# Optimization experiments

Measured on AMD Instinct MI355X. Metric: run time of the kernel, lower is better.

## Reference

```python
import jax, jax.numpy as jnp
import numpy as np

D = 1024  # in_features == latent_dim
EPS = 1e-5


def _layernorm(x, g, b):
    mu = jnp.mean(x, axis=-1, keepdims=True)
    var = jnp.mean(jnp.square(x - mu), axis=-1, keepdims=True)
    return (x - mu) * jax.lax.rsqrt(var + EPS) * g + b


def setup_inputs() -> dict:
    key = jax.random.key(0)
    ks = jax.random.split(key, 8)
    s = 1.0 / np.sqrt(D)
    return {
        "x": jax.random.normal(ks[0], (4, 4096, D), dtype=jnp.float32),
        "w_qkv": jax.random.uniform(ks[1], (3 * D, D), jnp.float32, -s, s),
        "w_o": jax.random.uniform(ks[2], (D, D), jnp.float32, -s, s),
        "w1": jax.random.uniform(ks[3], (D, D), jnp.float32, -s, s),
        "b1": jax.random.uniform(ks[4], (D,), jnp.float32, -s, s),
        "w2": jax.random.uniform(ks[5], (D, D), jnp.float32, -s, s),
        "b2": jax.random.uniform(ks[6], (D,), jnp.float32, -s, s),
        "ln1_g": jnp.ones((D,), jnp.float32),
        "ln1_b": jnp.zeros((D,), jnp.float32),
        "ln2_g": jnp.ones((D,), jnp.float32),
        "ln2_b": jnp.zeros((D,), jnp.float32),
    }


def reference(x, w_qkv, w_o, w1, b1, w2, b2, ln1_g, ln1_b, ln2_g, ln2_b):
    B, S, _ = x.shape
    scale = 1.0 / np.sqrt(D * 1)  # 1/sqrt(latent_dim * n_heads), n_heads=1
    qkv = jnp.einsum("bsd,ed->bse", x, w_qkv)            # [B,S,3D]
    qkv = qkv.reshape(B, S, 1, 3 * D).transpose(0, 2, 1, 3)  # [B,1,S,3D]
    q, k, v = jnp.split(qkv, 3, axis=-1)                  # each [B,1,S,D]
    logits = jnp.einsum("bhid,bhjd->bhij", q, k) * scale  # [B,1,S,S]
    # Faithful quirk: softmax over the HEAD axis (dim=1). With 1 head this
    # yields an all-ones attention matrix.
    attn = jax.nn.softmax(logits, axis=1)
    vals = jnp.einsum("bhij,bhjd->bhid", attn, v)         # [B,1,S,D]
    vals = vals.transpose(0, 2, 1, 3).reshape(B, S, D)
    attn_out = jnp.einsum("bsd,ed->bse", vals, w_o)
    # squeeze(-2) is a no-op for S>1
    x = _layernorm(x + attn_out, ln1_g, ln1_b)
    h = jax.nn.gelu(jnp.einsum("bsd,ed->bse", x, w1) + b1, approximate=False)
    mlp_out = jnp.einsum("bsd,ed->bse", h, w2) + b2
    return _layernorm(x + mlp_out, ln2_g, ln2_b)
```

## Files before the change

### kernel.cpp

```cpp
#include <hip/hip_runtime.h>
#include <hip/hip_bf16.h>

typedef __hip_bfloat16 bf16;
typedef __attribute__((ext_vector_type(8))) short short8;
typedef __attribute__((ext_vector_type(4))) float f32x4;

#define DDIM 1024
#define SEQ  4096
#define NB   4
#define MTOT (NB*SEQ)

static __device__ __forceinline__ unsigned short f2bf(float f) {
    __hip_bfloat16 h = __float2bfloat16(f);
    unsigned short u; __builtin_memcpy(&u, &h, 2); return u;
}
static __device__ __forceinline__ float bf2f(unsigned short u) {
    __hip_bfloat16 h; __builtin_memcpy(&h, &u, 2); return __bfloat162float(h);
}

__global__ __launch_bounds__(256) void pack_w_kernel(
    const float* __restrict__ w1, const float* __restrict__ w2,
    short8* __restrict__ w1p, short8* __restrict__ w2p)
{
    int gid  = blockIdx.x*256 + threadIdx.x;
    int m    = gid >> 17;
    int id   = gid & 131071;
    int frag = id >> 6, lane = id & 63;
    int ntile = frag >> 5, kt32 = frag & 31;
    int n = ntile*16 + (lane & 15);
    int k = kt32*32 + (lane >> 4)*8;
    const float* src = (m ? w2 : w1) + (size_t)n*DDIM + k;
    float4 a = *(const float4*)src;
    float4 b = *(const float4*)(src + 4);
    short8 o;
    o[0]=(short)f2bf(a.x); o[1]=(short)f2bf(a.y); o[2]=(short)f2bf(a.z); o[3]=(short)f2bf(a.w);
    o[4]=(short)f2bf(b.x); o[5]=(short)f2bf(b.y); o[6]=(short)f2bf(b.z); o[7]=(short)f2bf(b.w);
    (m ? w2p : w1p)[id] = o;
}

__global__ __launch_bounds__(256) void colsum_partial_kernel(
    const float* __restrict__ x, float* __restrict__ partial)
{
    int d  = blockIdx.x*256 + threadIdx.x;
    int b  = blockIdx.y;
    int sl = blockIdx.z;
    const float* p = x + ((size_t)b*SEQ + (size_t)sl*128)*DDIM + d;
    float s = 0.f;
    #pragma unroll 4
    for (int i = 0; i < 128; ++i) s += p[(size_t)i*DDIM];
    partial[((size_t)sl*NB + b)*DDIM + d] = s;
}

__global__ __launch_bounds__(256) void colsum_reduce_kernel(
    const float* __restrict__ partial, float* __restrict__ xsum)
{
    int d = blockIdx.x*256 + threadIdx.x;
    int b = blockIdx.y;
    float s = 0.f;
    #pragma unroll
    for (int sl = 0; sl < 32; ++sl) s += partial[((size_t)sl*NB + b)*DDIM + d];
    xsum[b*DDIM + d] = s;
}

__global__ __launch_bounds__(256) void matvec_kernel(
    const float* __restrict__ W, const float* __restrict__ vin, float* __restrict__ vout)
{
    int b = blockIdx.y;
    int g = threadIdx.x >> 4;
    int t = threadIdx.x & 15;
    int e = blockIdx.x*16 + g;
    const float* w = W + (size_t)e*DDIM;
    const float* v = vin + b*DDIM;
    float s = 0.f;
    for (int k = t; k < DDIM; k += 16) s += w[k]*v[k];
    #pragma unroll
    for (int o = 8; o; o >>= 1) s += __shfl_down(s, o, 16);
    if (t == 0) vout[b*DDIM + e] = s;
}

__global__ __launch_bounds__(256) void ln1_kernel(
    const float* __restrict__ x, const float* __restrict__ avec,
    const float* __restrict__ g1, const float* __restrict__ b1,
    unsigned short* __restrict__ x1b)
{
    int row = blockIdx.x;
    int b   = row >> 12;
    int tid = threadIdx.x;
    const float4* xr = (const float4*)(x + (size_t)row*DDIM);
    const float4* av = (const float4*)(avec + (size_t)b*DDIM);
    float4 xv = xr[tid], a4 = av[tid];
    float y0 = xv.x+a4.x, y1 = xv.y+a4.y, y2 = xv.z+a4.z, y3 = xv.w+a4.w;
    float s  = y0+y1+y2+y3;
    float ss = y0*y0+y1*y1+y2*y2+y3*y3;
    #pragma unroll
    for (int o = 32; o; o >>= 1) { s += __shfl_down(s,o,64); ss += __shfl_down(ss,o,64); }
    __shared__ float red[8];
    if ((tid&63) == 0) { red[tid>>6] = s; red[4+(tid>>6)] = ss; }
    __syncthreads();
    float St = red[0]+red[1]+red[2]+red[3];
    float Sq = red[4]+red[5]+red[6]+red[7];
    float mu = St*(1.0f/DDIM);
    float rs = rsqrtf(Sq*(1.0f/DDIM) - mu*mu + 1e-5f);
    float4 g4 = ((const float4*)g1)[tid];
    float4 bb = ((const float4*)b1)[tid];
    ushort4 o;
    o.x = f2bf((y0-mu)*rs*g4.x + bb.x);
    o.y = f2bf((y1-mu)*rs*g4.y + bb.y);
    o.z = f2bf((y2-mu)*rs*g4.z + bb.z);
    o.w = f2bf((y3-mu)*rs*g4.w + bb.w);
    *(ushort4*)(x1b + (size_t)row*DDIM + tid*4) = o;
}

template<int MODE>
__global__ __launch_bounds__(256, 2) void gemm_bp_kernel(
    const bf16* __restrict__ A, const short8* __restrict__ Bp,
    const float* __restrict__ bias, const unsigned short* __restrict__ resid,
    unsigned short* __restrict__ outb, float* __restrict__ outf)
{
    constexpr int K = 1024, N = 1024, BK = 64, NT = K / BK;
    __shared__ __align__(16) bf16 lds[2][128*BK];
    const int tid  = threadIdx.x;
    const int wave = tid >> 6, lane = tid & 63;

    int bid = blockIdx.x;
    int swz = (bid & 7) * 128 + (bid >> 3);
    const size_t bm = (size_t)(swz >> 3) * 128;
    const size_t bn = (size_t)(swz & 7) * 128;

    const int wm = wave >> 1;
    const int wn = wave & 1;

    const int srow = tid >> 3;
    const int skel = (((tid & 7) ^ ((tid >> 3) & 7)) << 3);

    const int fr = lane & 15;
    const int fs = lane >> 4;
    int foff[2];
    #pragma unroll
    for (int ks = 0; ks < 2; ++ks)
        foff[ks] = fr*128 + (((ks*4 + fs) ^ (fr & 7)) << 4);

    const bf16* Ab = A + bm * K;
    const int nt0 = (int)(bn >> 4) + wn*4;

    auto stageA = [&](int b, int kt) {
        #pragma unroll
        for (int g = 0; g < 4; ++g) {
            const bf16* gp = Ab + (size_t)(g*32 + srow) * K + kt*BK + skel;
            __builtin_amdgcn_global_load_lds(
                (const __attribute__((address_space(1))) void*)gp,
                (__attribute__((address_space(3))) void*)
                    ((char*)&lds[b][0] + g*4096 + wave*1024),
                16, 0, 0);
        }
    };
    auto loadB = [&](int kt, short8* bf_) {
        #pragma unroll
        for (int kk = 0; kk < 2; ++kk)
            #pragma unroll
            for (int nf = 0; nf < 4; ++nf)
                bf_[kk*4 + nf] = Bp[((nt0 + nf)*32 + kt*2 + kk)*64 + lane];
    };

    f32x4 acc[4][4] = {};
    short8 bcur[8], bnxt[8];

    stageA(0, 0);
    loadB(0, bcur);

    auto iter = [&](int t, short8* bc, short8* bn_) {
        if (t < NT-1) {
            stageA((t+1) & 1, t+1);
            asm volatile("s_waitcnt vmcnt(4)" ::: "memory");
        } else {
            asm volatile("s_waitcnt vmcnt(0)" ::: "memory");
        }
        __builtin_amdgcn_s_barrier();
        if (t < NT-1) {
            loadB(t+1, bn_);
            asm volatile("" ::: "memory");
        }
        const char* LA = (const char*)&lds[t & 1][0] + wm*8192;
        #pragma unroll
        for (int ks = 0; ks < 2; ++ks) {
            short8 af[4];
            #pragma unroll
            for (int m = 0; m < 4; ++m) af[m] = *(const short8*)(LA + m*2048 + foff[ks]);
            __builtin_amdgcn_s_setprio(1);
            #pragma unroll
            for (int m = 0; m < 4; ++m)
                #pragma unroll
                for (int n = 0; n < 4; ++n)
                    acc[m][n] = __builtin_amdgcn_mfma_f32_16x16x32_bf16(
                        af[m], bc[ks*4 + n], acc[m][n], 0, 0, 0);
            __builtin_amdgcn_s_setprio(0);
        }
        __builtin_amdgcn_s_barrier();
    };

    #pragma unroll
    for (int t = 0; t < NT; t += 2) {
        iter(t,   bcur, bnxt);
        iter(t+1, bnxt, bcur);
    }

    const int crow = (lane >> 4) * 4, ccol = lane & 15;
    #pragma unroll
    for (int n = 0; n < 4; ++n) {
        size_t col = bn + wn*64 + n*16 + ccol;
        float bv = bias[col];
        #pragma unroll
        for (int m = 0; m < 4; ++m) {
            #pragma unroll
            for (int r = 0; r < 4; ++r) {
                size_t row = bm + wm*64 + m*16 + crow + r;
                float v = acc[m][n][r] + bv;
                if (MODE == 1) {
                    float ge = 0.5f*v*(1.0f + erff(v*0.70710678118f));
                    outb[row*(size_t)N + col] = f2bf(ge);
                } else {
                    outf[row*(size_t)N + col] = v + bf2f(resid[row*(size_t)N + col]);
                }
            }
        }
    }
}

__global__ __launch_bounds__(256) void ln2_kernel(
    float* __restrict__ out, const float* __restrict__ g2, const float* __restrict__ b2)
{
    int row = blockIdx.x;
    int tid = threadIdx.x;
    float4* orow = (float4*)(out + (size_t)row*DDIM);
    float4 y = orow[tid];
    float s  = y.x+y.y+y.z+y.w;
    float ss = y.x*y.x+y.y*y.y+y.z*y.z+y.w*y.w;
    #pragma unroll
    for (int o = 32; o; o >>= 1) { s += __shfl_down(s,o,64); ss += __shfl_down(ss,o,64); }
    __shared__ float red[8];
    if ((tid&63) == 0) { red[tid>>6] = s; red[4+(tid>>6)] = ss; }
    __syncthreads();
    float St = red[0]+red[1]+red[2]+red[3];
    float Sq = red[4]+red[5]+red[6]+red[7];
    float mu = St*(1.0f/DDIM);
    float rs = rsqrtf(Sq*(1.0f/DDIM) - mu*mu + 1e-5f);
    float4 g4 = ((const float4*)g2)[tid];
    float4 bb = ((const float4*)b2)[tid];
    float4 n;
    n.x = (y.x-mu)*rs*g4.x + bb.x;
    n.y = (y.y-mu)*rs*g4.y + bb.y;
    n.z = (y.z-mu)*rs*g4.z + bb.z;
    n.w = (y.w-mu)*rs*g4.w + bb.w;
    orow[tid] = n;
}

extern "C" void kernel_launch(void* const* d_in, const int* in_sizes, int n_in,
                              void* d_out, int out_size, void* d_ws, size_t ws_size,
                              hipStream_t stream)
{
    const float* x     = (const float*)d_in[0];
    const float* w_qkv = (const float*)d_in[1];
    const float* w_o   = (const float*)d_in[2];
    const float* w1    = (const float*)d_in[3];
    const float* b1    = (const float*)d_in[4];
    const float* w2    = (const float*)d_in[5];
    const float* b2    = (const float*)d_in[6];
    const float* ln1g  = (const float*)d_in[7];
    const float* ln1b  = (const float*)d_in[8];
    const float* ln2g  = (const float*)d_in[9];
    const float* ln2b  = (const float*)d_in[10];
    float* out = (float*)d_out;
    char* ws = (char*)d_ws;

    unsigned short* x1b = (unsigned short*)(ws);
    unsigned short* hb  = (unsigned short*)(ws + 33554432);
    short8* w1p = (short8*)(ws + 67108864);
    short8* w2p = (short8*)(ws + 69206016);
    float* partial = (float*)(ws + 71303168);
    float* xsum    = (float*)(ws + 71827456);
    float* tvec    = (float*)(ws + 71843840);
    float* avec    = (float*)(ws + 71860224);

    pack_w_kernel<<<dim3(1024), 256, 0, stream>>>(w1, w2, w1p, w2p);
    colsum_partial_kernel<<<dim3(4, NB, 32), 256, 0, stream>>>(x, partial);
    colsum_reduce_kernel<<<dim3(4, NB), 256, 0, stream>>>(partial, xsum);
    matvec_kernel<<<dim3(64, NB), 256, 0, stream>>>(w_qkv + (size_t)2*DDIM*DDIM, xsum, tvec);
    matvec_kernel<<<dim3(64, NB), 256, 0, stream>>>(w_o, tvec, avec);
    ln1_kernel<<<dim3(MTOT), 256, 0, stream>>>(x, avec, ln1g, ln1b, x1b);
    gemm_bp_kernel<1><<<dim3(1024), 256, 0, stream>>>(
        (const bf16*)x1b, w1p, b1, nullptr, hb, nullptr);
    gemm_bp_kernel<2><<<dim3(1024), 256, 0, stream>>>(
        (const bf16*)hb, w2p, b2, x1b, nullptr, out);
    ln2_kernel<<<dim3(MTOT), 256, 0, stream>>>(out, ln2g, ln2b);
}
```

Measured before the change: 187.2 us.

## Use full-width 64-row GEMM tiles and fuse LayerNorm2 into the second GEMM

```diff
diff --git a/kernel.cpp b/kernel.cpp
--- a/kernel.cpp
+++ b/kernel.cpp
@@ -26,9 +26,9 @@
     int m    = gid >> 17;
     int id   = gid & 131071;
     int frag = id >> 6, lane = id & 63;
-    int ntile = frag >> 5, kt32 = frag & 31;
+    int ntile = frag >> 5, k32 = frag & 31;
     int n = ntile*16 + (lane & 15);
-    int k = kt32*32 + (lane >> 4)*8;
+    int k = k32*32 + (lane >> 4)*8;
     const float* src = (m ? w2 : w1) + (size_t)n*DDIM + k;
     float4 a = *(const float4*)src;
     float4 b = *(const float4*)(src + 4);
@@ -112,146 +112,164 @@
 }
 
 template<int MODE>
-__global__ __launch_bounds__(256, 2) void gemm_bp_kernel(
+__global__ __launch_bounds__(512, 2) void gemm_fw_kernel(
     const bf16* __restrict__ A, const short8* __restrict__ Bp,
     const float* __restrict__ bias, const unsigned short* __restrict__ resid,
-    unsigned short* __restrict__ outb, float* __restrict__ outf)
-{
-    constexpr int K = 1024, N = 1024, BK = 64, NT = K / BK;
-    __shared__ __align__(16) bf16 lds[2][128*BK];
+    unsigned short* __restrict__ outb, float* __restrict__ outf,
+    const float* __restrict__ lng, const float* __restrict__ lnb)
+{
+    extern __shared__ char smem[];
     const int tid  = threadIdx.x;
     const int wave = tid >> 6, lane = tid & 63;
-
-    int bid = blockIdx.x;
-    int swz = (bid & 7) * 128 + (bid >> 3);
-    const size_t bm = (size_t)(swz >> 3) * 128;
-    const size_t bn = (size_t)(swz & 7) * 128;
-
-    const int wm = wave >> 1;
-    const int wn = wave & 1;
-
-    const int srow = tid >> 3;
-    const int skel = (((tid & 7) ^ ((tid >> 3) & 7)) << 3);
-
-    const int fr = lane & 15;
-    const int fs = lane >> 4;
-    int foff[2];
-    #pragma unroll
-    for (int ks = 0; ks < 2; ++ks)
-        foff[ks] = fr*128 + (((ks*4 + fs) ^ (fr & 7)) << 4);
-
-    const bf16* Ab = A + bm * K;
-    const int nt0 = (int)(bn >> 4) + wn*4;
-
-    auto stageA = [&](int b, int kt) {
-        #pragma unroll
-        for (int g = 0; g < 4; ++g) {
-            const bf16* gp = Ab + (size_t)(g*32 + srow) * K + kt*BK + skel;
+    const size_t bm = (size_t)blockIdx.x * 64;
+    const bf16* Ab = A + bm * DDIM;
+
+    auto stageA = [&](int seg) {
+        #pragma unroll
+        for (int i = 0; i < 4; ++i) {
+            int row = i*16 + wave*2 + (lane >> 5);
+            int sl  = (lane & 31) ^ (row & 7);
+            const bf16* gp = Ab + (size_t)row*DDIM + seg*256 + sl*8;
             __builtin_amdgcn_global_load_lds(
                 (const __attribute__((address_space(1))) void*)gp,
                 (__attribute__((address_space(3))) void*)
-                    ((char*)&lds[b][0] + g*4096 + wave*1024),
+                    (smem + seg*32768 + i*8192 + wave*1024),
                 16, 0, 0);
         }
     };
-    auto loadB = [&](int kt, short8* bf_) {
-        #pragma unroll
-        for (int kk = 0; kk < 2; ++kk)
-            #pragma unroll
-            for (int nf = 0; nf < 4; ++nf)
-                bf_[kk*4 + nf] = Bp[((nt0 + nf)*32 + kt*2 + kk)*64 + lane];
+
+    const int nt0 = wave * 8;
+    auto loadB = [&](int k32, short8* bf_) {
+        #pragma unroll
+        for (int nf = 0; nf < 8; ++nf)
+            bf_[nf] = Bp[((size_t)(nt0 + nf)*32 + k32)*64 + lane];
     };
 
-    f32x4 acc[4][4] = {};
-    short8 bcur[8], bnxt[8];
-
-    stageA(0, 0);
-    loadB(0, bcur);
-
-    auto iter = [&](int t, short8* bc, short8* bn_) {
-        if (t < NT-1) {
-            stageA((t+1) & 1, t+1);
-            asm volatile("s_waitcnt vmcnt(4)" ::: "memory");
-        } else {
-            asm volatile("s_waitcnt vmcnt(0)" ::: "memory");
-        }
-        __builtin_amdgcn_s_barrier();
-        if (t < NT-1) {
-            loadB(t+1, bn_);
-            asm volatile("" ::: "memory");
-        }
-        const char* LA = (const char*)&lds[t & 1][0] + wm*8192;
-        #pragma unroll
-        for (int ks = 0; ks < 2; ++ks) {
-            short8 af[4];
-            #pragma unroll
-            for (int m = 0; m < 4; ++m) af[m] = *(const short8*)(LA + m*2048 + foff[ks]);
-            __builtin_amdgcn_s_setprio(1);
-            #pragma unroll
-            for (int m = 0; m < 4; ++m)
-                #pragma unroll
-                for (int n = 0; n < 4; ++n)
-                    acc[m][n] = __builtin_amdgcn_mfma_f32_16x16x32_bf16(
-                        af[m], bc[ks*4 + n], acc[m][n], 0, 0, 0);
-            __builtin_amdgcn_s_setprio(0);
-        }
-        __builtin_amdgcn_s_barrier();
+    const int fr = lane & 15, fs = lane >> 4, q = lane >> 4;
+    f32x4 acc[4][8] = {};
+
+    auto compute = [&](int k32, short8* bf_) {
+        const char* base = smem + (k32 >> 3)*32768;
+        short8 af[4];
+        #pragma unroll
+        for (int mf = 0; mf < 4; ++mf) {
+            int R = mf*16 + fr;
+            int phys = ((k32 & 7)*4 + fs) ^ (R & 7);
+            af[mf] = *(const short8*)(base + R*512 + phys*16);
+        }
+        __builtin_amdgcn_s_setprio(1);
+        #pragma unroll
+        for (int mf = 0; mf < 4; ++mf)
+            #pragma unroll
+            for (int nf = 0; nf < 8; ++nf)
+                acc[mf][nf] = __builtin_amdgcn_mfma_f32_16x16x32_bf16(
+                    af[mf], bf_[nf], acc[mf][nf], 0, 0, 0);
+        __builtin_amdgcn_s_setprio(0);
     };
 
-    #pragma unroll
-    for (int t = 0; t < NT; t += 2) {
-        iter(t,   bcur, bnxt);
-        iter(t+1, bnxt, bcur);
+    short8 bA[8], bB[8];
+    stageA(0);
+    loadB(0, bA);
+    __syncthreads();
+
+    for (int seg = 0; seg < 4; ++seg) {
+        if (seg < 3) stageA(seg + 1);
+        #pragma unroll
+        for (int j = 0; j < 8; j += 2) {
+            int k = seg*8 + j;
+            if (k + 1 < 32) loadB(k + 1, bB);
+            compute(k, bA);
+            if (k + 2 < 32) loadB(k + 2, bA);
+            compute(k + 1, bB);
+        }
+        __syncthreads();
     }
 
-    const int crow = (lane >> 4) * 4, ccol = lane & 15;
-    #pragma unroll
-    for (int n = 0; n < 4; ++n) {
-        size_t col = bn + wn*64 + n*16 + ccol;
-        float bv = bias[col];
-        #pragma unroll
-        for (int m = 0; m < 4; ++m) {
-            #pragma unroll
-            for (int r = 0; r < 4; ++r) {
-                size_t row = bm + wm*64 + m*16 + crow + r;
-                float v = acc[m][n][r] + bv;
-                if (MODE == 1) {
+    if (MODE == 1) {
+        #pragma unroll
+        for (int nf = 0; nf < 8; ++nf) {
+            size_t col = (size_t)wave*128 + nf*16 + fr;
+            float bv = bias[col];
+            #pragma unroll
+            for (int mf = 0; mf < 4; ++mf)
+                #pragma unroll
+                for (int rr = 0; rr < 4; ++rr) {
+                    size_t row = bm + mf*16 + q*4 + rr;
+                    float v = acc[mf][nf][rr] + bv;
                     float ge = 0.5f*v*(1.0f + erff(v*0.70710678118f));
-                    outb[row*(size_t)N + col] = f2bf(ge);
-                } else {
-                    outf[row*(size_t)N + col] = v + bf2f(resid[row*(size_t)N + col]);
+                    outb[row*DDIM + col] = f2bf(ge);
+                }
+        }
+    } else {
+        float bv[8];
+        #pragma unroll
+        for (int nf = 0; nf < 8; ++nf) bv[nf] = bias[(size_t)wave*128 + nf*16 + fr];
+        float vs[4][4] = {}, vq[4][4] = {};
+        #pragma unroll
+        for (int mf = 0; mf < 4; ++mf)
+            #pragma unroll
+            for (int rr = 0; rr < 4; ++rr) {
+                size_t row = bm + mf*16 + q*4 + rr;
+                #pragma unroll
+                for (int nf = 0; nf < 8; ++nf) {
+                    size_t col = (size_t)wave*128 + nf*16 + fr;
+                    float v = acc[mf][nf][rr] + bv[nf] + bf2f(resid[row*DDIM + col]);
+                    acc[mf][nf][rr] = v;
+                    vs[mf][rr] += v;
+                    vq[mf][rr] += v*v;
                 }
             }
-        }
+        #pragma unroll
+        for (int o = 1; o < 16; o <<= 1) {
+            #pragma unroll
+            for (int mf = 0; mf < 4; ++mf)
+                #pragma unroll
+                for (int rr = 0; rr < 4; ++rr) {
+                    vs[mf][rr] += __shfl_xor(vs[mf][rr], o);
+                    vq[mf][rr] += __shfl_xor(vq[mf][rr], o);
+                }
+        }
+        float* lred = (float*)smem;
+        if (fr == 0) {
+            #pragma unroll
+            for (int mf = 0; mf < 4; ++mf)
+                #pragma unroll
+                for (int rr = 0; rr < 4; ++rr) {
+                    int R = mf*16 + q*4 + rr;
+                    lred[(wave*64 + R)*2]     = vs[mf][rr];
+                    lred[(wave*64 + R)*2 + 1] = vq[mf][rr];
+                }
+        }
+        __syncthreads();
+        float* lpar = (float*)(smem + 4096);
+        if (tid < 64) {
+            float s = 0.f, sq = 0.f;
+            #pragma unroll
+            for (int w = 0; w < 8; ++w) { s += lred[(w*64 + tid)*2]; sq += lred[(w*64 + tid)*2 + 1]; }
+            float mu = s * (1.0f/DDIM);
+            float rs = rsqrtf(sq * (1.0f/DDIM) - mu*mu + 1e-5f);
+            lpar[tid*2] = mu; lpar[tid*2 + 1] = rs;
+        }
+        __syncthreads();
+        float g2c[8], b2c[8];
+        #pragma unroll
+        for (int nf = 0; nf < 8; ++nf) {
+            size_t col = (size_t)wave*128 + nf*16 + fr;
+            g2c[nf] = lng[col]; b2c[nf] = lnb[col];
+        }
+        #pragma unroll
+        for (int mf = 0; mf < 4; ++mf)
+            #pragma unroll
+            for (int rr = 0; rr < 4; ++rr) {
+                int R = mf*16 + q*4 + rr;
+                float mu = lpar[R*2], rs = lpar[R*2 + 1];
+                #pragma unroll
+                for (int nf = 0; nf < 8; ++nf) {
+                    size_t col = (size_t)wave*128 + nf*16 + fr;
+                    outf[(bm + R)*DDIM + col] = (acc[mf][nf][rr] - mu)*rs*g2c[nf] + b2c[nf];
+                }
+            }
     }
-}
-
-__global__ __launch_bounds__(256) void ln2_kernel(
-    float* __restrict__ out, const float* __restrict__ g2, const float* __restrict__ b2)
-{
-    int row = blockIdx.x;
-    int tid = threadIdx.x;
-    float4* orow = (float4*)(out + (size_t)row*DDIM);
-    float4 y = orow[tid];
-    float s  = y.x+y.y+y.z+y.w;
-    float ss = y.x*y.x+y.y*y.y+y.z*y.z+y.w*y.w;
-    #pragma unroll
-    for (int o = 32; o; o >>= 1) { s += __shfl_down(s,o,64); ss += __shfl_down(ss,o,64); }
-    __shared__ float red[8];
-    if ((tid&63) == 0) { red[tid>>6] = s; red[4+(tid>>6)] = ss; }
-    __syncthreads();
-    float St = red[0]+red[1]+red[2]+red[3];
-    float Sq = red[4]+red[5]+red[6]+red[7];
-    float mu = St*(1.0f/DDIM);
-    float rs = rsqrtf(Sq*(1.0f/DDIM) - mu*mu + 1e-5f);
-    float4 g4 = ((const float4*)g2)[tid];
-    float4 bb = ((const float4*)b2)[tid];
-    float4 n;
-    n.x = (y.x-mu)*rs*g4.x + bb.x;
-    n.y = (y.y-mu)*rs*g4.y + bb.y;
-    n.z = (y.z-mu)*rs*g4.z + bb.z;
-    n.w = (y.w-mu)*rs*g4.w + bb.w;
-    orow[tid] = n;
 }
 
 extern "C" void kernel_launch(void* const* d_in, const int* in_sizes, int n_in,
@@ -281,15 +299,19 @@
     float* tvec    = (float*)(ws + 71843840);
     float* avec    = (float*)(ws + 71860224);
 
+    (void)hipFuncSetAttribute((const void*)gemm_fw_kernel<1>,
+                              hipFuncAttributeMaxDynamicSharedMemorySize, 131072);
+    (void)hipFuncSetAttribute((const void*)gemm_fw_kernel<2>,
+                              hipFuncAttributeMaxDynamicSharedMemorySize, 131072);
+
     pack_w_kernel<<<dim3(1024), 256, 0, stream>>>(w1, w2, w1p, w2p);
     colsum_partial_kernel<<<dim3(4, NB, 32), 256, 0, stream>>>(x, partial);
     colsum_reduce_kernel<<<dim3(4, NB), 256, 0, stream>>>(partial, xsum);
     matvec_kernel<<<dim3(64, NB), 256, 0, stream>>>(w_qkv + (size_t)2*DDIM*DDIM, xsum, tvec);
     matvec_kernel<<<dim3(64, NB), 256, 0, stream>>>(w_o, tvec, avec);
     ln1_kernel<<<dim3(MTOT), 256, 0, stream>>>(x, avec, ln1g, ln1b, x1b);
-    gemm_bp_kernel<1><<<dim3(1024), 256, 0, stream>>>(
-        (const bf16*)x1b, w1p, b1, nullptr, hb, nullptr);
-    gemm_bp_kernel<2><<<dim3(1024), 256, 0, stream>>>(
-        (const bf16*)hb, w2p, b2, x1b, nullptr, out);
-    ln2_kernel<<<dim3(MTOT), 256, 0, stream>>>(out, ln2g, ln2b);
-}
+    gemm_fw_kernel<1><<<dim3(256), 512, 131072, stream>>>(
+        (const bf16*)x1b, w1p, b1, nullptr, hb, nullptr, nullptr, nullptr);
+    gemm_fw_kernel<2><<<dim3(256), 512, 131072, stream>>>(
+        (const bf16*)hb, w2p, b2, x1b, nullptr, out, ln2g, ln2b);
+}
```

After: 218.1 us. +16.5%, slower.
